# Kernel tuning notes

Measured on AMD Instinct MI355X. Metric: run time of the kernel, lower is better.

## Reference

```python
import jax, jax.numpy as jnp
import numpy as np
from jax import lax

T = 20.0
DT = 0.1
TAU_M = 20.0
TAU_S = 5.0
STEPS = int(T / DT)  # 200
BATCH, IN_DIM, OUT_DIM = 512, 784, 10


def setup_inputs() -> dict:
    key = jax.random.key(0)
    k1, k2 = jax.random.split(key)
    x = (jax.random.uniform(k1, (BATCH, IN_DIM, STEPS)) < 0.02).astype(jnp.float32)
    # nn.init.normal_(weight, mu=0.1, std=0.1)
    w = 0.1 + 0.1 * jax.random.normal(k2, (OUT_DIM, IN_DIM), dtype=jnp.float32)
    return {"input": x, "weight": w}


def _snn_forward(input, weight):
    """SpikingLinear.manual_forward (eval mode) + FirstSpikeTime.forward."""
    B, _, steps = input.shape
    O = weight.shape[0]
    a_m = 1.0 - DT / TAU_M
    a_s = 1.0 - DT / TAU_S
    # precompute all per-step synaptic drives: F.linear(input[:,:,i-1], W)
    drive = jnp.einsum('bit,oi->tbo', input[:, :, :steps - 1], weight)  # [steps-1,B,O]

    def step(carry, drv):
        V, I = carry
        Vn = a_m * V + (DT / TAU_M) * I
        In = a_s * I + drv
        spk = (Vn > 1.0).astype(input.dtype)
        return ((1.0 - spk) * Vn, In), (spk, In)  # reset V where spiked

    zero = jnp.zeros((B, O), input.dtype)
    _, (spk, Iseq) = lax.scan(step, (zero, zero), drive)
    pad = jnp.zeros((1, B, O), input.dtype)
    output = jnp.moveaxis(jnp.concatenate([pad, spk], 0), 0, 2)  # [B,O,steps], step0 = 0
    I_full = jnp.moveaxis(jnp.concatenate([pad, Iseq], 0), 0, 2)

    # FirstSpikeTime: argmax of (steps..1) * spikes -> index of first spike
    idx = jnp.arange(steps, 0, -1, dtype=input.dtype)
    fst = jnp.argmax(idx[None, None, :] * output, axis=2)  # [B,O] int (0 if silent)
    out = jnp.where(fst == 0, steps - 1, fst).astype(jnp.float32)
    return out, (I_full, output, fst)


def reference(input, weight):
    out, _ = _snn_forward(input, weight)
    return out
```

## Files before the change

kernel.cpp:

```cpp
#include <hip/hip_runtime.h>

#define STEPS   200
#define NT      199
#define BATCH   512
#define IN_DIM  784
#define OUT_DIM 10
#define NCHUNK  16
#define CHUNK   49
#define WSTR    12
#define DROW    200
#define NC2     8

__global__ __launch_bounds__(1024, 4) void snn_fwd(
    const float* __restrict__ x,
    const float* __restrict__ w,
    float* __restrict__ out)
{
    __shared__ float smem[NC2 * OUT_DIM * DROW];
    float* w_lds = smem;
    float* dlds  = smem;

    const int b    = blockIdx.x;
    const int tid  = threadIdx.x;
    const int c    = tid >> 6;
    const int lane = tid & 63;
    const int t0   = lane * 4;
    const bool active = (t0 < STEPS);

    for (int idx = tid; idx < IN_DIM * OUT_DIM; idx += 1024) {
        int o = idx / IN_DIM;
        int i = idx - o * IN_DIM;
        w_lds[i * WSTR + o] = w[idx];
    }
    __syncthreads();

    float2 acc[4][5];
    #pragma unroll
    for (int q = 0; q < 4; ++q)
        #pragma unroll
        for (int j = 0; j < 5; ++j) acc[q][j] = make_float2(0.0f, 0.0f);

    if (active) {
        const float* xb = x + (size_t)b * IN_DIM * STEPS + t0;
        const int i0 = c * CHUNK;

        #define LD(ii) (*(const float4*)(xb + (size_t)(ii) * STEPS))
        #define CONSUME(xv, ii)                                                  \
            do {                                                                 \
                const float4 w0 = *(const float4*)&w_lds[(ii) * WSTR + 0];       \
                const float4 w1 = *(const float4*)&w_lds[(ii) * WSTR + 4];       \
                const float2 w2 = *(const float2*)&w_lds[(ii) * WSTR + 8];       \
                const float xq[4] = {(xv).x, (xv).y, (xv).z, (xv).w};            \
                _Pragma("unroll")                                                \
                for (int q = 0; q < 4; ++q) {                                    \
                    acc[q][0].x = fmaf(xq[q], w0.x, acc[q][0].x);                \
                    acc[q][0].y = fmaf(xq[q], w0.y, acc[q][0].y);                \
                    acc[q][1].x = fmaf(xq[q], w0.z, acc[q][1].x);                \
                    acc[q][1].y = fmaf(xq[q], w0.w, acc[q][1].y);                \
                    acc[q][2].x = fmaf(xq[q], w1.x, acc[q][2].x);                \
                    acc[q][2].y = fmaf(xq[q], w1.y, acc[q][2].y);                \
                    acc[q][3].x = fmaf(xq[q], w1.z, acc[q][3].x);                \
                    acc[q][3].y = fmaf(xq[q], w1.w, acc[q][3].y);                \
                    acc[q][4].x = fmaf(xq[q], w2.x, acc[q][4].x);                \
                    acc[q][4].y = fmaf(xq[q], w2.y, acc[q][4].y);                \
                }                                                                \
            } while (0)

        float4 X0 = LD(i0 + 0), X1 = LD(i0 + 1), X2 = LD(i0 + 2), X3 = LD(i0 + 3);
        for (int j = 0; j < 11; ++j) {
            const int r = i0 + 4 * j;
            float4 N0 = LD(r + 4), N1 = LD(r + 5), N2 = LD(r + 6), N3 = LD(r + 7);
            CONSUME(X0, r + 0);
            CONSUME(X1, r + 1);
            CONSUME(X2, r + 2);
            CONSUME(X3, r + 3);
            X0 = N0; X1 = N1; X2 = N2; X3 = N3;
        }
        {
            float4 L = LD(i0 + 48);
            CONSUME(X0, i0 + 44);
            CONSUME(X1, i0 + 45);
            CONSUME(X2, i0 + 46);
            CONSUME(X3, i0 + 47);
            CONSUME(L,  i0 + 48);
        }
        #undef LD
        #undef CONSUME
    }

    __syncthreads();

    const int c2 = c >> 1;
    if (active && !(c & 1)) {
        #pragma unroll
        for (int j = 0; j < 5; ++j) {
            float4 v0 = make_float4(acc[0][j].x, acc[1][j].x, acc[2][j].x, acc[3][j].x);
            float4 v1 = make_float4(acc[0][j].y, acc[1][j].y, acc[2][j].y, acc[3][j].y);
            *(float4*)&dlds[((c2 * OUT_DIM + 2 * j    ) * DROW) + t0] = v0;
            *(float4*)&dlds[((c2 * OUT_DIM + 2 * j + 1) * DROW) + t0] = v1;
        }
    }
    __syncthreads();
    if (active && (c & 1)) {
        #pragma unroll
        for (int j = 0; j < 5; ++j) {
            float* r0 = &dlds[((c2 * OUT_DIM + 2 * j    ) * DROW) + t0];
            float* r1 = &dlds[((c2 * OUT_DIM + 2 * j + 1) * DROW) + t0];
            float4 v0 = *(float4*)r0;
            float4 v1 = *(float4*)r1;
            v0.x += acc[0][j].x; v0.y += acc[1][j].x; v0.z += acc[2][j].x; v0.w += acc[3][j].x;
            v1.x += acc[0][j].y; v1.y += acc[1][j].y; v1.z += acc[2][j].y; v1.w += acc[3][j].y;
            *(float4*)r0 = v0;
            *(float4*)r1 = v1;
        }
    }
    __syncthreads();

    if (tid < OUT_DIM) {
        const int o = tid;
        const float a_m = 0.995f;
        const float b_m = 0.005f;
        const float a_s = 0.98f;

        float V = 0.0f, I = 0.0f;
        int fst = 0;
        for (int s = 0; s < NT; ++s) {
            float drv = 0.0f;
            #pragma unroll
            for (int k = 0; k < NC2; ++k)
                drv += dlds[(k * OUT_DIM + o) * DROW + s];
            float Vn = a_m * V + b_m * I;
            I = a_s * I + drv;
            if (Vn > 1.0f) {
                if (fst == 0) fst = s + 1;
                V = 0.0f;
            } else {
                V = Vn;
            }
        }
        out[b * OUT_DIM + o] = (fst == 0) ? (float)(STEPS - 1) : (float)fst;
    }
}

extern "C" void kernel_launch(void* const* d_in, const int* in_sizes, int n_in,
                              void* d_out, int out_size, void* d_ws, size_t ws_size,
                              hipStream_t stream) {
    const float* x = (const float*)d_in[0];
    const float* w = (const float*)d_in[1];
    float* out = (float*)d_out;
    snn_fwd<<<dim3(BATCH), dim3(1024), 0, stream>>>(x, w, out);
}
```

Measured before the change: 445.4 us.

## Split SNN into multi-block drive kernel and separate scan kernel

Splits the single fused kernel into two. The first computes partial synaptic drives, with four 256-thread blocks per batch item each covering a quarter of the input rows, and writes the partials to workspace. The second kernel sums the four partials into shared memory and runs the serial membrane scan. The aim is finer-grained blocks and a serial scan that no longer holds a 1024-thread block idle. The cost is a global-memory round trip for the partials and an extra kernel launch.

```diff
diff --git a/kernel.cpp b/kernel.cpp
--- a/kernel.cpp
+++ b/kernel.cpp
@@ -5,32 +5,32 @@
 #define BATCH   512
 #define IN_DIM  784
 #define OUT_DIM 10
-#define NCHUNK  16
-#define CHUNK   49
+#define NQ      4
+#define QROWS   196
+#define WROWS   49
 #define WSTR    12
-#define DROW    200
-#define NC2     8
 
-__global__ __launch_bounds__(1024, 4) void snn_fwd(
+__global__ __launch_bounds__(256) void snn_drive(
     const float* __restrict__ x,
     const float* __restrict__ w,
-    float* __restrict__ out)
+    float* __restrict__ dpart)
 {
-    __shared__ float smem[NC2 * OUT_DIM * DROW];
-    float* w_lds = smem;
-    float* dlds  = smem;
+    __shared__ float w_lds[QROWS * WSTR];
+    __shared__ float pw[4 * OUT_DIM * STEPS];
 
-    const int b    = blockIdx.x;
+    const int bid  = blockIdx.x;
+    const int b    = bid >> 2;
+    const int rq   = bid & 3;
     const int tid  = threadIdx.x;
-    const int c    = tid >> 6;
+    const int wv   = tid >> 6;
     const int lane = tid & 63;
     const int t0   = lane * 4;
-    const bool active = (t0 < STEPS);
+    const int rowbase = rq * QROWS;
 
-    for (int idx = tid; idx < IN_DIM * OUT_DIM; idx += 1024) {
-        int o = idx / IN_DIM;
-        int i = idx - o * IN_DIM;
-        w_lds[i * WSTR + o] = w[idx];
+    for (int idx = tid; idx < QROWS * OUT_DIM; idx += 256) {
+        int o = idx / QROWS;
+        int i = idx - o * QROWS;
+        w_lds[i * WSTR + o] = w[o * IN_DIM + rowbase + i];
     }
     __syncthreads();
 
@@ -40,16 +40,16 @@
         #pragma unroll
         for (int j = 0; j < 5; ++j) acc[q][j] = make_float2(0.0f, 0.0f);
 
-    if (active) {
-        const float* xb = x + (size_t)b * IN_DIM * STEPS + t0;
-        const int i0 = c * CHUNK;
+    if (t0 < STEPS) {
+        const float* xb = x + (size_t)b * IN_DIM * STEPS + (size_t)rowbase * STEPS + t0;
+        const int i0 = wv * WROWS;
 
-        #define LD(ii) (*(const float4*)(xb + (size_t)(ii) * STEPS))
-        #define CONSUME(xv, ii)                                                  \
+        #define LD(r) (*(const float4*)(xb + (size_t)(r) * STEPS))
+        #define CONSUME(xv, r)                                                   \
             do {                                                                 \
-                const float4 w0 = *(const float4*)&w_lds[(ii) * WSTR + 0];       \
-                const float4 w1 = *(const float4*)&w_lds[(ii) * WSTR + 4];       \
-                const float2 w2 = *(const float2*)&w_lds[(ii) * WSTR + 8];       \
+                const float4 w0 = *(const float4*)&w_lds[(r) * WSTR + 0];        \
+                const float4 w1 = *(const float4*)&w_lds[(r) * WSTR + 4];        \
+                const float2 w2 = *(const float2*)&w_lds[(r) * WSTR + 8];        \
                 const float xq[4] = {(xv).x, (xv).y, (xv).z, (xv).w};            \
                 _Pragma("unroll")                                                \
                 for (int q = 0; q < 4; ++q) {                                    \
@@ -86,38 +86,61 @@
         }
         #undef LD
         #undef CONSUME
-    }
 
-    __syncthreads();
-
-    const int c2 = c >> 1;
-    if (active && !(c & 1)) {
         #pragma unroll
         for (int j = 0; j < 5; ++j) {
             float4 v0 = make_float4(acc[0][j].x, acc[1][j].x, acc[2][j].x, acc[3][j].x);
             float4 v1 = make_float4(acc[0][j].y, acc[1][j].y, acc[2][j].y, acc[3][j].y);
-            *(float4*)&dlds[((c2 * OUT_DIM + 2 * j    ) * DROW) + t0] = v0;
-            *(float4*)&dlds[((c2 * OUT_DIM + 2 * j + 1) * DROW) + t0] = v1;
-        }
-    }
-    __syncthreads();
-    if (active && (c & 1)) {
-        #pragma unroll
-        for (int j = 0; j < 5; ++j) {
-            float* r0 = &dlds[((c2 * OUT_DIM + 2 * j    ) * DROW) + t0];
-            float* r1 = &dlds[((c2 * OUT_DIM + 2 * j + 1) * DROW) + t0];
-            float4 v0 = *(float4*)r0;
-            float4 v1 = *(float4*)r1;
-            v0.x += acc[0][j].x; v0.y += acc[1][j].x; v0.z += acc[2][j].x; v0.w += acc[3][j].x;
-            v1.x += acc[0][j].y; v1.y += acc[1][j].y; v1.z += acc[2][j].y; v1.w += acc[3][j].y;
-            *(float4*)r0 = v0;
-            *(float4*)r1 = v1;
+            *(float4*)&pw[(wv * OUT_DIM + 2 * j    ) * STEPS + t0] = v0;
+            *(float4*)&pw[(wv * OUT_DIM + 2 * j + 1) * STEPS + t0] = v1;
         }
     }
     __syncthreads();
 
-    if (tid < OUT_DIM) {
-        const int o = tid;
+    float* dst = dpart + ((size_t)(rq * BATCH + b)) * OUT_DIM * STEPS;
+    const float4* p0 = (const float4*)&pw[0 * OUT_DIM * STEPS];
+    const float4* p1 = (const float4*)&pw[1 * OUT_DIM * STEPS];
+    const float4* p2 = (const float4*)&pw[2 * OUT_DIM * STEPS];
+    const float4* p3 = (const float4*)&pw[3 * OUT_DIM * STEPS];
+    for (int s = tid; s < OUT_DIM * STEPS / 4; s += 256) {
+        float4 a = p0[s], c = p1[s], d = p2[s], e = p3[s];
+        float4 v;
+        v.x = ((a.x + c.x) + d.x) + e.x;
+        v.y = ((a.y + c.y) + d.y) + e.y;
+        v.z = ((a.z + c.z) + d.z) + e.z;
+        v.w = ((a.w + c.w) + d.w) + e.w;
+        ((float4*)dst)[s] = v;
+    }
+}
+
+__global__ __launch_bounds__(64) void snn_scan(
+    const float* __restrict__ dpart,
+    float* __restrict__ out)
+{
+    __shared__ float ds[OUT_DIM * STEPS];
+
+    const int b    = blockIdx.x;
+    const int lane = threadIdx.x;
+    const size_t qstride4 = (size_t)BATCH * OUT_DIM * STEPS / 4;
+    const float4* base = (const float4*)(dpart + (size_t)b * OUT_DIM * STEPS);
+
+    for (int s = lane; s < OUT_DIM * STEPS / 4; s += 64) {
+        float4 a = base[s];
+        float4 c = base[s + qstride4];
+        float4 d = base[s + 2 * qstride4];
+        float4 e = base[s + 3 * qstride4];
+        float4 v;
+        v.x = ((a.x + c.x) + d.x) + e.x;
+        v.y = ((a.y + c.y) + d.y) + e.y;
+        v.z = ((a.z + c.z) + d.z) + e.z;
+        v.w = ((a.w + c.w) + d.w) + e.w;
+        ((float4*)ds)[s] = v;
+    }
+    __syncthreads();
+
+    if (lane < OUT_DIM) {
+        const int o = lane;
+        const float* dso = &ds[o * STEPS];
         const float a_m = 0.995f;
         const float b_m = 0.005f;
         const float a_s = 0.98f;
@@ -125,10 +148,7 @@
         float V = 0.0f, I = 0.0f;
         int fst = 0;
         for (int s = 0; s < NT; ++s) {
-            float drv = 0.0f;
-            #pragma unroll
-            for (int k = 0; k < NC2; ++k)
-                drv += dlds[(k * OUT_DIM + o) * DROW + s];
+            float drv = dso[s];
             float Vn = a_m * V + b_m * I;
             I = a_s * I + drv;
             if (Vn > 1.0f) {
@@ -147,6 +167,9 @@
                               hipStream_t stream) {
     const float* x = (const float*)d_in[0];
     const float* w = (const float*)d_in[1];
-    float* out = (float*)d_out;
-    snn_fwd<<<dim3(BATCH), dim3(1024), 0, stream>>>(x, w, out);
+    float* out   = (float*)d_out;
+    float* dpart = (float*)d_ws;
+
+    snn_drive<<<dim3(BATCH * NQ), dim3(256), 0, stream>>>(x, w, dpart);
+    snn_scan <<<dim3(BATCH),      dim3(64),  0, stream>>>(dpart, out);
 }
```

After: 443.0 us. No clear change (-0.5%).
